# Kernel optimization log

Hardware: AMD Instinct MI355X
Metric: run time of the kernel (lower is better)

## Reference

```python
import jax, jax.numpy as jnp
import numpy as np

CK, CV, CS = 8, 120, 64          # key / value / spatial-basis channels
NUM_AGENTS, NQ_PER = 4, 4        # queries chunked per agent; chunk(a,4) hard-codes NQ_PER=4
HID = 256                        # lstm_hidden_size
NA = 18                          # num_actions
U = 8                            # Fourier freqs; CS = U*U = 64
MLP_W = 512                      # q/a mlp hidden width


def spatial_basis(h, w):
    # fixed (h, w, CS) cos-product Fourier basis (SpatialBasis buffer)
    ph = jnp.arange(1, h + 1, dtype=jnp.float32)[:, None] * jnp.ones((1, w), jnp.float32) * (np.pi / h)
    pw = jnp.ones((h, 1), jnp.float32) * jnp.arange(1, w + 1, dtype=jnp.float32)[None, :] * (np.pi / w)
    u = jnp.arange(1, U + 1, dtype=jnp.float32)
    ca = jnp.cos(ph[..., None] * u)   # (h, w, U)
    cb = jnp.cos(pw[..., None] * u)   # (h, w, U)
    return jnp.einsum('hwu,hwv->hwuv', ca, cb).reshape(h, w, U * U)


def mlp3(x, w0, b0, w1, b1, w2, b2):
    # build_mlp with 2 relu hidden layers + identity output
    x = jax.nn.relu(x @ w0 + b0)
    x = jax.nn.relu(x @ w1 + b1)
    return x @ w2 + b2


def lstm_cell(x, h, c, w_ih, w_hh, b_ih, b_hh):
    gates = x @ w_ih.T + b_ih + h @ w_hh.T + b_hh
    i, f, g, o = jnp.split(gates, 4, axis=1)
    c2 = jax.nn.sigmoid(f) * c + jax.nn.sigmoid(i) * jnp.tanh(g)
    return jax.nn.sigmoid(o) * jnp.tanh(c2), c2


def setup_inputs() -> dict:
    key = jax.random.key(0)
    ks = jax.random.split(key, 24)
    n, h, w = 128, 64, 64
    s = 0.02
    nq = NUM_AGENTS * NQ_PER
    q_out = nq * (CK + CS)                       # 1152
    a_in = NQ_PER * (CK + 2 * CS + CV) + 2       # 1026
    r = lambda k, shp: jax.random.normal(k, shp, jnp.float32)
    return {
        'x': r(ks[0], (n, h, w, CK + CV)),
        'c': 1,
        'r_prev': r(ks[1], (n,)),
        'a_prev': r(ks[2], (n,)),
        'prev_hidden': r(ks[3], (n, HID)),
        'prev_cell': r(ks[4], (n, HID)),
        'q_w0': r(ks[5], (HID, MLP_W)) * s, 'q_b0': jnp.zeros((MLP_W,), jnp.float32),
        'q_w1': r(ks[6], (MLP_W, MLP_W)) * s, 'q_b1': jnp.zeros((MLP_W,), jnp.float32),
        'q_w2': r(ks[7], (MLP_W, q_out)) * s, 'q_b2': jnp.zeros((q_out,), jnp.float32),
        'a_w0': r(ks[8], (a_in, MLP_W)) * s, 'a_b0': jnp.zeros((MLP_W,), jnp.float32),
        'a_w1': r(ks[9], (MLP_W, MLP_W)) * s, 'a_b1': jnp.zeros((MLP_W,), jnp.float32),
        'a_w2': r(ks[10], (MLP_W, HID)) * s, 'a_b2': jnp.zeros((HID,), jnp.float32),
        'w_ih': r(ks[11], (4 * HID, HID)) * s, 'w_hh': r(ks[12], (4 * HID, HID)) * s,
        'b_ih': jnp.zeros((4 * HID,), jnp.float32), 'b_hh': jnp.zeros((4 * HID,), jnp.float32),
        'p_w': r(ks[13], (HID, NA)) * s, 'p_b': jnp.zeros((NA,), jnp.float32),
        'v_w': r(ks[14], (HID, NA)) * s, 'v_b': jnp.zeros((NA,), jnp.float32),
    }


def reference(x, c, r_prev, a_prev, prev_hidden, prev_cell,
              q_w0, q_b0, q_w1, q_b1, q_w2, q_b2,
              a_w0, a_b0, a_w1, a_b1, a_w2, a_b2,
              w_ih, w_hh, b_ih, b_hh, p_w, p_b, v_w, v_b):
    n, h, w, _ = x.shape
    S = spatial_basis(h, w)
    Sb = jnp.broadcast_to(S, (n, h, w, CS))
    K = jnp.concatenate([x[..., :CK], Sb], axis=-1)   # (n,h,w,CK+CS)
    V = jnp.concatenate([x[..., CK:], Sb], axis=-1)   # (n,h,w,CV+CS)
    # queries from previous hidden state, take agent c's chunk
    Q = mlp3(prev_hidden, q_w0, q_b0, q_w1, q_b1, q_w2, q_b2)
    Q = Q.reshape(n, NUM_AGENTS * NQ_PER, CK + CS)[:, c * NQ_PER:(c + 1) * NQ_PER, :]  # (n,4,CK+CS)
    # spatial QK attention with softmax over the h*w grid
    A = jnp.einsum('nhwd,nqd->nhwq', K, Q)            # (n,h,w,4)
    A = jax.nn.softmax(A.reshape(n, h * w, NQ_PER), axis=1).reshape(n, h, w, NQ_PER)
    a = jnp.einsum('nhwq,nhwd->nqd', A, V)            # (n,4,CV+CS)
    # concat answers + queries + prev reward/action scalars
    answer = jnp.concatenate([a.reshape(n, -1), Q.reshape(n, -1),
                              r_prev[:, None], a_prev[:, None]], axis=1)  # (n,1026)
    answer = mlp3(answer, a_w0, a_b0, a_w1, a_b1, a_w2, a_b2)             # (n,HID)
    hN, _cN = lstm_cell(answer, prev_hidden, prev_cell, w_ih, w_hh, b_ih, b_hh)
    logits = hN @ p_w + p_b
    values = hN @ v_w + v_b
    return logits, values
```

## Files before the change

### kernel.cpp

```cpp
#include <hip/hip_runtime.h>
#include <math.h>

#define NTOT   128
#define NPOS   4096
#define PVCH   16
#define PVLEN  256
#define LCH    8
#define LCLEN  512

__global__ __launch_bounds__(256) void k_gemm(
    const float* __restrict__ Ad, const float* __restrict__ pA,
    const float* __restrict__ biasA, int nzA, int reluA,
    const float* __restrict__ pvR, const float* __restrict__ scl,
    const float* __restrict__ W, float* __restrict__ pbuf,
    int N, int K, int ldw, int gkc, const int* __restrict__ cptr, int cmul) {
  __shared__ float Xs[4][128];
  const int t  = threadIdx.x;
  const int j  = blockIdx.x * 256 + t;
  const int m0 = blockIdx.y * 4;
  const int k0 = blockIdx.z * gkc;
  const int klen = min(gkc, K - k0);
  const int coff = cptr[0] * cmul;

  for (int idx = t; idx < 4 * klen; idx += 256) {
    int mi = idx / klen;
    int kk = idx - mi * klen;
    int col = k0 + kk;
    float s;
    if (Ad) {
      bool pv = false;
      int q = 0, d = 0;
      if (pvR && col < 736) {
        q = col / 184; d = col - q * 184;
        pv = (d < 120);
      }
      if (pv) {
        const size_t eo = (size_t)(m0 + mi) * 480 + q * 120 + d;
        float s0 = 0.f, s1 = 0.f, s2 = 0.f, s3 = 0.f;
#pragma unroll
        for (int c = 0; c < PVCH; c += 4) {
          s0 += pvR[(size_t)((c + 0) * NTOT) * 480 + eo];
          s1 += pvR[(size_t)((c + 1) * NTOT) * 480 + eo];
          s2 += pvR[(size_t)((c + 2) * NTOT) * 480 + eo];
          s3 += pvR[(size_t)((c + 3) * NTOT) * 480 + eo];
        }
        s = ((s0 + s1) + (s2 + s3)) * scl[(size_t)(m0 + mi) * 4 + q];
      } else {
        s = Ad[(size_t)(m0 + mi) * K + col];
      }
    } else {
      float s0 = biasA[col], s1 = 0.f, s2 = 0.f, s3 = 0.f;
      int z = 0;
      for (; z + 4 <= nzA; z += 4) {
        s0 += pA[((size_t)(z + 0) * NTOT + m0 + mi) * K + col];
        s1 += pA[((size_t)(z + 1) * NTOT + m0 + mi) * K + col];
        s2 += pA[((size_t)(z + 2) * NTOT + m0 + mi) * K + col];
        s3 += pA[((size_t)(z + 3) * NTOT + m0 + mi) * K + col];
      }
      for (; z < nzA; ++z) s0 += pA[((size_t)z * NTOT + m0 + mi) * K + col];
      s = (s0 + s1) + (s2 + s3);
      if (reluA) s = fmaxf(s, 0.f);
    }
    Xs[mi][kk] = s;
  }
  __syncthreads();

  if (j < N) {
    float acc[4];
#pragma unroll
    for (int mi = 0; mi < 4; ++mi) acc[mi] = 0.f;
    const float* wp = W + (size_t)k0 * ldw + coff + j;
#pragma unroll 16
    for (int kk = 0; kk < klen; ++kk) {
      float wv = wp[(size_t)kk * ldw];
#pragma unroll
      for (int mi = 0; mi < 4; ++mi) acc[mi] = fmaf(Xs[mi][kk], wv, acc[mi]);
    }
    float* op = pbuf + ((size_t)blockIdx.z * NTOT + m0) * N + j;
#pragma unroll
    for (int mi = 0; mi < 4; ++mi) op[(size_t)mi * N] = acc[mi];
  }
}

__global__ __launch_bounds__(512) void k_logits(
    const float* __restrict__ x, const float* __restrict__ pQ,
    const float* __restrict__ q_b2, const int* __restrict__ cptr,
    const float* __restrict__ r_prev, const float* __restrict__ a_prev,
    float* __restrict__ Pw, float* __restrict__ Lpart,
    float* __restrict__ rsum, float* __restrict__ ans) {
  const int ck = blockIdx.x;
  const int n  = blockIdx.y;
  const int t  = threadIdx.x;
  const int wave = t >> 6, lane = t & 63;

  __shared__ float Qs[4][72];
  __shared__ float ct[64][8];
  __shared__ float cbQ[4 * 576];
  __shared__ float4 wlds[LCLEN];
  __shared__ float red[4][8];

  const float PI64 = 3.14159265358979323846f / 64.f;

  if (t < 288) {
    const int coff = cptr[0] * 288;
    float s = q_b2[coff + t];
#pragma unroll
    for (int z = 0; z < 8; ++z) s += pQ[((size_t)z * NTOT + n) * 288 + t];
    Qs[t / 72][t % 72] = s;
  }
  {
    int i = t >> 3, u = t & 7;
    ct[i][u] = cosf((float)((i + 1) * (u + 1)) * PI64);
  }
  __syncthreads();

  for (int e = t; e < 2048; e += 512) {
    int q = e >> 9, j = (e >> 3) & 63, u = e & 7;
    float s = 0.f;
#pragma unroll
    for (int v = 0; v < 8; ++v) s += ct[j][v] * Qs[q][8 + u * 8 + v];
    cbQ[q * 576 + j * 9 + u] = s;
  }
  __syncthreads();

  const int base = ck * LCLEN;
  const float* xp = x + (size_t)n * NPOS * 128;

  const int irow = ck * 8 + wave;
  {
    const int pos = base + t;
    const float4* xr = reinterpret_cast<const float4*>(xp + (size_t)pos * 128);
    float4 xa = xr[0], xb = xr[1];
    float4 w;
    float lg[4];
#pragma unroll
    for (int q = 0; q < 4; ++q) {
      float s = xa.x * Qs[q][0] + xa.y * Qs[q][1] + xa.z * Qs[q][2] + xa.w * Qs[q][3]
              + xb.x * Qs[q][4] + xb.y * Qs[q][5] + xb.z * Qs[q][6] + xb.w * Qs[q][7];
      const float* cq = cbQ + q * 576 + lane * 9;
      float s2 = 0.f;
#pragma unroll
      for (int u = 0; u < 8; ++u) s2 += ct[irow][u] * cq[u];
      lg[q] = s + s2;
    }
    w.x = __expf(lg[0]); w.y = __expf(lg[1]);
    w.z = __expf(lg[2]); w.w = __expf(lg[3]);
    wlds[t] = w;
    reinterpret_cast<float4*>(Pw)[(size_t)n * NPOS + base + t] = w;

    float lsum[4] = {w.x, w.y, w.z, w.w};
#pragma unroll
    for (int off = 32; off; off >>= 1)
#pragma unroll
      for (int q = 0; q < 4; ++q) lsum[q] += __shfl_xor(lsum[q], off);
    if (lane == 0)
#pragma unroll
      for (int q = 0; q < 4; ++q) red[q][wave] = lsum[q];
  }
  __syncthreads();
  if (t < 4) {
    float s = 0.f;
#pragma unroll
    for (int w8 = 0; w8 < 8; ++w8) s += red[t][w8];
    Lpart[((size_t)n * LCH + ck) * 4 + t] = s;
  }

  if (t < 256) {
    int i = t >> 5, q = (t >> 3) & 3, v = t & 7;
    const float* wb = reinterpret_cast<const float*>(&wlds[i * 64]) + q;
    float s0 = 0.f, s1 = 0.f, s2 = 0.f, s3 = 0.f;
#pragma unroll 8
    for (int j = 0; j < 64; j += 4) {
      s0 += wb[(j + 0) * 4] * ct[j + 0][v];
      s1 += wb[(j + 1) * 4] * ct[j + 1][v];
      s2 += wb[(j + 2) * 4] * ct[j + 2][v];
      s3 += wb[(j + 3) * 4] * ct[j + 3][v];
    }
    rsum[((size_t)n * 64 + ck * 8 + i) * 32 + q * 8 + v] = (s0 + s1) + (s2 + s3);
  }

  if (ck == 0) {
    float* ap = ans + (size_t)n * 1026;
    if (t < 288) ap[736 + t] = Qs[t / 72][t % 72];
    if (t == 288) { ap[1024] = r_prev[n]; ap[1025] = a_prev[n]; }
  }
}

__global__ __launch_bounds__(256, 4) void k_pv(
    const float* __restrict__ x, const float* __restrict__ Pw,
    const float* __restrict__ Lpart, const float* __restrict__ rsum,
    float* __restrict__ pvp, float* __restrict__ scl, float* __restrict__ ans) {
  const int n = blockIdx.y, ck = blockIdx.x;
  const int t = threadIdx.x, wave = t >> 6, lane = t & 63;
  __shared__ float4 wl[PVLEN];
  __shared__ __align__(16) float part[4][4][120];
  __shared__ float ct2[64][8];
  __shared__ float sc_s[4];

  const int base = ck * PVLEN;
  wl[t] = reinterpret_cast<const float4*>(Pw)[(size_t)n * NPOS + base + t];
  __syncthreads();

  const int xl = (lane < 60) ? lane : 59;
  const float* vb = x + ((size_t)n * NPOS + base + wave * 64) * 128 + 8 + 2 * xl;

  float ax0[4] = {0.f, 0.f, 0.f, 0.f};
  float ax1[4] = {0.f, 0.f, 0.f, 0.f};
#pragma unroll
  for (int b = 0; b < 4; ++b) {
    float2 v0  = *reinterpret_cast<const float2*>(vb + (size_t)(b * 16 + 0)  * 128);
    float2 v1  = *reinterpret_cast<const float2*>(vb + (size_t)(b * 16 + 1)  * 128);
    float2 v2  = *reinterpret_cast<const float2*>(vb + (size_t)(b * 16 + 2)  * 128);
    float2 v3  = *reinterpret_cast<const float2*>(vb + (size_t)(b * 16 + 3)  * 128);
    float2 v4  = *reinterpret_cast<const float2*>(vb + (size_t)(b * 16 + 4)  * 128);
    float2 v5  = *reinterpret_cast<const float2*>(vb + (size_t)(b * 16 + 5)  * 128);
    float2 v6  = *reinterpret_cast<const float2*>(vb + (size_t)(b * 16 + 6)  * 128);
    float2 v7  = *reinterpret_cast<const float2*>(vb + (size_t)(b * 16 + 7)  * 128);
    float2 v8  = *reinterpret_cast<const float2*>(vb + (size_t)(b * 16 + 8)  * 128);
    float2 v9  = *reinterpret_cast<const float2*>(vb + (size_t)(b * 16 + 9)  * 128);
    float2 v10 = *reinterpret_cast<const float2*>(vb + (size_t)(b * 16 + 10) * 128);
    float2 v11 = *reinterpret_cast<const float2*>(vb + (size_t)(b * 16 + 11) * 128);
    float2 v12 = *reinterpret_cast<const float2*>(vb + (size_t)(b * 16 + 12) * 128);
    float2 v13 = *reinterpret_cast<const float2*>(vb + (size_t)(b * 16 + 13) * 128);
    float2 v14 = *reinterpret_cast<const float2*>(vb + (size_t)(b * 16 + 14) * 128);
    float2 v15 = *reinterpret_cast<const float2*>(vb + (size_t)(b * 16 + 15) * 128);
#define ACC(VV, II)                                                              \
    {                                                                            \
      float4 w = wl[wave * 64 + b * 16 + II];                                    \
      ax0[0] += w.x * VV.x; ax1[0] += w.x * VV.y;                                \
      ax0[1] += w.y * VV.x; ax1[1] += w.y * VV.y;                                \
      ax0[2] += w.z * VV.x; ax1[2] += w.z * VV.y;                                \
      ax0[3] += w.w * VV.x; ax1[3] += w.w * VV.y;                                \
    }
    ACC(v0, 0)  ACC(v1, 1)  ACC(v2, 2)  ACC(v3, 3)
    ACC(v4, 4)  ACC(v5, 5)  ACC(v6, 6)  ACC(v7, 7)
    ACC(v8, 8)  ACC(v9, 9)  ACC(v10, 10) ACC(v11, 11)
    ACC(v12, 12) ACC(v13, 13) ACC(v14, 14) ACC(v15, 15)
#undef ACC
  }
  if (lane < 60) {
#pragma unroll
    for (int q = 0; q < 4; ++q)
      *reinterpret_cast<float2*>(&part[wave][q][2 * lane]) = make_float2(ax0[q], ax1[q]);
  }
  __syncthreads();

  float* op = pvp + ((size_t)ck * NTOT + n) * 480;
  for (int idx = t; idx < 480; idx += 256) {
    const int q = idx / 120, d = idx - q * 120;
    op[idx] = (part[0][q][d] + part[1][q][d]) + (part[2][q][d] + part[3][q][d]);
  }

  if (ck == 0) {
    const float PI64 = 3.14159265358979323846f / 64.f;
    if (t < 4) {
      float L = 0.f;
#pragma unroll
      for (int c = 0; c < LCH; ++c) L += Lpart[((size_t)n * LCH + c) * 4 + t];
      float s = 1.f / L;
      scl[(size_t)n * 4 + t] = s;
      sc_s[t] = s;
    }
    for (int e = t; e < 512; e += 256) {
      int i = e >> 3, u = e & 7;
      ct2[i][u] = cosf((float)((i + 1) * (u + 1)) * PI64);
    }
    __syncthreads();
    {
      const int q = t >> 6, uv = t & 63, u = uv >> 3, v = uv & 7;
      const float* rp = rsum + (size_t)n * 64 * 32 + q * 8 + v;
      float s0 = 0.f, s1 = 0.f, s2 = 0.f, s3 = 0.f;
#pragma unroll 8
      for (int row = 0; row < 64; row += 4) {
        s0 += ct2[row + 0][u] * rp[(row + 0) * 32];
        s1 += ct2[row + 1][u] * rp[(row + 1) * 32];
        s2 += ct2[row + 2][u] * rp[(row + 2) * 32];
        s3 += ct2[row + 3][u] * rp[(row + 3) * 32];
      }
      ans[(size_t)n * 1026 + q * 184 + 120 + uv] = sc_s[q] * ((s0 + s1) + (s2 + s3));
    }
  }
}

__global__ __launch_bounds__(256) void k_gates(
    const float* __restrict__ pA, const float* __restrict__ biasA,
    const float* __restrict__ hp,
    const float* __restrict__ w_ih, const float* __restrict__ w_hh,
    const float* __restrict__ b_ih, const float* __restrict__ b_hh,
    float* __restrict__ gbuf) {
  const int t = threadIdx.x;
  const int n0 = blockIdx.x * 2;
  const int r0 = blockIdx.y * 64;
  __shared__ float xs[2][256], hs[2][256];
  __shared__ float red[64][4][5];
#pragma unroll
  for (int s = 0; s < 2; ++s) {
    float v0 = biasA[t], v1 = 0.f, v2 = 0.f, v3 = 0.f;
#pragma unroll
    for (int z = 0; z < 8; z += 4) {
      v0 += pA[((size_t)(z + 0) * NTOT + n0 + s) * 256 + t];
      v1 += pA[((size_t)(z + 1) * NTOT + n0 + s) * 256 + t];
      v2 += pA[((size_t)(z + 2) * NTOT + n0 + s) * 256 + t];
      v3 += pA[((size_t)(z + 3) * NTOT + n0 + s) * 256 + t];
    }
    xs[s][t] = (v0 + v1) + (v2 + v3);
    hs[s][t] = hp[(size_t)(n0 + s) * 256 + t];
  }
  __syncthreads();
  const int r = t >> 2, kq = t & 3;
  const int row = r0 + r;
  const float4* wi = reinterpret_cast<const float4*>(w_ih + (size_t)row * 256 + kq * 64);
  const float4* wh = reinterpret_cast<const float4*>(w_hh + (size_t)row * 256 + kq * 64);
  float s00 = 0.f, s01 = 0.f, s10 = 0.f, s11 = 0.f;
#pragma unroll
  for (int i = 0; i < 16; ++i) {
    float4 a = wi[i], b = wh[i];
    const int k4 = kq * 64 + i * 4;
    s00 += a.x * xs[0][k4] + a.y * xs[0][k4 + 1] + a.z * xs[0][k4 + 2] + a.w * xs[0][k4 + 3];
    s01 += a.x * xs[1][k4] + a.y * xs[1][k4 + 1] + a.z * xs[1][k4 + 2] + a.w * xs[1][k4 + 3];
    s10 += b.x * hs[0][k4] + b.y * hs[0][k4 + 1] + b.z * hs[0][k4 + 2] + b.w * hs[0][k4 + 3];
    s11 += b.x * hs[1][k4] + b.y * hs[1][k4 + 1] + b.z * hs[1][k4 + 2] + b.w * hs[1][k4 + 3];
  }
  red[r][kq][0] = s00; red[r][kq][1] = s01; red[r][kq][2] = s10; red[r][kq][3] = s11;
  __syncthreads();
  if (t < 128) {
    const int rr = t >> 1, s = t & 1;
    float g = b_ih[r0 + rr] + b_hh[r0 + rr];
#pragma unroll
    for (int k = 0; k < 4; ++k) g += red[rr][k][s] + red[rr][k][2 + s];
    gbuf[(size_t)(n0 + s) * 1024 + r0 + rr] = g;
  }
}

__global__ __launch_bounds__(256) void k_lstm2(
    const float* __restrict__ gbuf, const float* __restrict__ cp,
    const float* __restrict__ p_w, const float* __restrict__ p_b,
    const float* __restrict__ v_w, const float* __restrict__ v_b,
    float* __restrict__ out) {
  const int t = threadIdx.x;
  const int n0 = blockIdx.x * 2;
  __shared__ float h2[2][256];
#pragma unroll
  for (int s = 0; s < 2; ++s) {
    const size_t gb = (size_t)(n0 + s) * 1024;
    float gi = gbuf[gb + t], gf = gbuf[gb + 256 + t];
    float gg = gbuf[gb + 512 + t], go = gbuf[gb + 768 + t];
    float si = 1.f / (1.f + __expf(-gi));
    float sf = 1.f / (1.f + __expf(-gf));
    float so = 1.f / (1.f + __expf(-go));
    float c2 = sf * cp[(size_t)(n0 + s) * 256 + t] + si * tanhf(gg);
    h2[s][t] = so * tanhf(c2);
  }
  __syncthreads();
  if (t < 72) {
    const int si = t / 36, r = t % 36, iv = r / 18, j = r % 18;
    const float* W = iv ? v_w : p_w;
    const float* B = iv ? v_b : p_b;
    float s = B[j];
#pragma unroll 8
    for (int k = 0; k < 256; ++k) s += h2[si][k] * W[k * 18 + j];
    out[(size_t)iv * (NTOT * 18) + (size_t)(n0 + si) * 18 + j] = s;
  }
}

extern "C" void kernel_launch(void* const* d_in, const int* in_sizes, int n_in,
                              void* d_out, int out_size, void* d_ws, size_t ws_size,
                              hipStream_t stream) {
  const float* x      = (const float*)d_in[0];
  const int*   cptr   = (const int*)d_in[1];
  const float* r_prev = (const float*)d_in[2];
  const float* a_prev = (const float*)d_in[3];
  const float* hprev  = (const float*)d_in[4];
  const float* cprev  = (const float*)d_in[5];
  const float* q_w0 = (const float*)d_in[6];
  const float* q_b0 = (const float*)d_in[7];
  const float* q_w1 = (const float*)d_in[8];
  const float* q_b1 = (const float*)d_in[9];
  const float* q_w2 = (const float*)d_in[10];
  const float* q_b2 = (const float*)d_in[11];
  const float* a_w0 = (const float*)d_in[12];
  const float* a_b0 = (const float*)d_in[13];
  const float* a_w1 = (const float*)d_in[14];
  const float* a_b1 = (const float*)d_in[15];
  const float* a_w2 = (const float*)d_in[16];
  const float* a_b2 = (const float*)d_in[17];
  const float* w_ih = (const float*)d_in[18];
  const float* w_hh = (const float*)d_in[19];
  const float* b_ih = (const float*)d_in[20];
  const float* b_hh = (const float*)d_in[21];
  const float* p_w  = (const float*)d_in[22];
  const float* p_b  = (const float*)d_in[23];
  const float* v_w  = (const float*)d_in[24];
  const float* v_b  = (const float*)d_in[25];
  float* out = (float*)d_out;
  float* ws  = (float*)d_ws;

  float* pQ   = ws;
  float* pb1  = pQ   + 294912;
  float* pb2  = pb1  + 589824;
  float* pb3  = pb2  + 524288;
  float* Pw   = pb3  + 262144;
  float* pvp  = Pw   + 2097152;
  float* ans  = pvp  + 983040;
  float* gbuf = ans  + 131328;
  float* Lp   = gbuf + 131072;
  float* rsum = Lp   + 4096;
  float* scl  = rsum + 262144;

  k_gemm<<<dim3(2, 32, 4), 256, 0, stream>>>(hprev, nullptr, nullptr, 0, 0, nullptr, nullptr,
                                             q_w0, pb1, 512, 256, 512, 64, cptr, 0);
  k_gemm<<<dim3(2, 32, 8), 256, 0, stream>>>(nullptr, pb1, q_b0, 4, 1, nullptr, nullptr,
                                             q_w1, pb2, 512, 512, 512, 64, cptr, 0);
  k_gemm<<<dim3(2, 32, 8), 256, 0, stream>>>(nullptr, pb2, q_b1, 8, 1, nullptr, nullptr,
                                             q_w2, pQ, 288, 512, 1152, 64, cptr, 288);

  k_logits<<<dim3(LCH, NTOT), 512, 0, stream>>>(x, pQ, q_b2, cptr, r_prev, a_prev,
                                                Pw, Lp, rsum, ans);
  k_pv<<<dim3(PVCH, NTOT), 256, 0, stream>>>(x, Pw, Lp, rsum, pvp, scl, ans);

  k_gemm<<<dim3(2, 32, 9), 256, 0, stream>>>(ans, nullptr, nullptr, 0, 0, pvp, scl,
                                             a_w0, pb1, 512, 1026, 512, 128, cptr, 0);
  k_gemm<<<dim3(2, 32, 8), 256, 0, stream>>>(nullptr, pb1, a_b0, 9, 1, nullptr, nullptr,
                                             a_w1, pb2, 512, 512, 512, 64, cptr, 0);
  k_gemm<<<dim3(1, 32, 8), 256, 0, stream>>>(nullptr, pb2, a_b1, 8, 1, nullptr, nullptr,
                                             a_w2, pb3, 256, 512, 256, 64, cptr, 0);

  k_gates<<<dim3(64, 16), 256, 0, stream>>>(pb3, a_b2, hprev, w_ih, w_hh, b_ih, b_hh, gbuf);
  k_lstm2<<<64, 256, 0, stream>>>(gbuf, cprev, p_w, p_b, v_w, v_b, out);
}
```

Measured before the change: 133.4 us.

## Fuse logits and PV into one attention kernel, drop Pw round-trip

The logits kernel and the PV-accumulation kernel are merged so the exponentiated weights stay in shared memory. This removes the global write and re-read of the weight buffer and a second pass over x. The cross-chunk finalisation moves into a small separate kernel. Each block now handles 512 positions with 8 waves instead of 256 positions, so there are fewer, larger blocks. Shared memory is reused between cbQ and the partial sums.

```diff
diff --git a/kernel.cpp b/kernel.cpp
--- a/kernel.cpp
+++ b/kernel.cpp
@@ -3,8 +3,7 @@
 
 #define NTOT   128
 #define NPOS   4096
-#define PVCH   16
-#define PVLEN  256
+#define PVCH   8
 #define LCH    8
 #define LCLEN  512
 
@@ -82,11 +81,11 @@
   }
 }
 
-__global__ __launch_bounds__(512) void k_logits(
+__global__ __launch_bounds__(512) void k_attn(
     const float* __restrict__ x, const float* __restrict__ pQ,
     const float* __restrict__ q_b2, const int* __restrict__ cptr,
     const float* __restrict__ r_prev, const float* __restrict__ a_prev,
-    float* __restrict__ Pw, float* __restrict__ Lpart,
+    float* __restrict__ pvp, float* __restrict__ Lpart,
     float* __restrict__ rsum, float* __restrict__ ans) {
   const int ck = blockIdx.x;
   const int n  = blockIdx.y;
@@ -95,9 +94,11 @@
 
   __shared__ float Qs[4][72];
   __shared__ float ct[64][8];
-  __shared__ float cbQ[4 * 576];
   __shared__ float4 wlds[LCLEN];
   __shared__ float red[4][8];
+  __shared__ __align__(16) float uni[3840];
+  float* cbQ = uni;
+  float (*part)[4][120] = reinterpret_cast<float (*)[4][120]>(uni);
 
   const float PI64 = 3.14159265358979323846f / 64.f;
 
@@ -125,8 +126,8 @@
 
   const int base = ck * LCLEN;
   const float* xp = x + (size_t)n * NPOS * 128;
-
   const int irow = ck * 8 + wave;
+
   {
     const int pos = base + t;
     const float4* xr = reinterpret_cast<const float4*>(xp + (size_t)pos * 128);
@@ -146,7 +147,6 @@
     w.x = __expf(lg[0]); w.y = __expf(lg[1]);
     w.z = __expf(lg[2]); w.w = __expf(lg[3]);
     wlds[t] = w;
-    reinterpret_cast<float4*>(Pw)[(size_t)n * NPOS + base + t] = w;
 
     float lsum[4] = {w.x, w.y, w.z, w.w};
 #pragma unroll
@@ -165,44 +165,8 @@
     Lpart[((size_t)n * LCH + ck) * 4 + t] = s;
   }
 
-  if (t < 256) {
-    int i = t >> 5, q = (t >> 3) & 3, v = t & 7;
-    const float* wb = reinterpret_cast<const float*>(&wlds[i * 64]) + q;
-    float s0 = 0.f, s1 = 0.f, s2 = 0.f, s3 = 0.f;
-#pragma unroll 8
-    for (int j = 0; j < 64; j += 4) {
-      s0 += wb[(j + 0) * 4] * ct[j + 0][v];
-      s1 += wb[(j + 1) * 4] * ct[j + 1][v];
-      s2 += wb[(j + 2) * 4] * ct[j + 2][v];
-      s3 += wb[(j + 3) * 4] * ct[j + 3][v];
-    }
-    rsum[((size_t)n * 64 + ck * 8 + i) * 32 + q * 8 + v] = (s0 + s1) + (s2 + s3);
-  }
-
-  if (ck == 0) {
-    float* ap = ans + (size_t)n * 1026;
-    if (t < 288) ap[736 + t] = Qs[t / 72][t % 72];
-    if (t == 288) { ap[1024] = r_prev[n]; ap[1025] = a_prev[n]; }
-  }
-}
-
-__global__ __launch_bounds__(256, 4) void k_pv(
-    const float* __restrict__ x, const float* __restrict__ Pw,
-    const float* __restrict__ Lpart, const float* __restrict__ rsum,
-    float* __restrict__ pvp, float* __restrict__ scl, float* __restrict__ ans) {
-  const int n = blockIdx.y, ck = blockIdx.x;
-  const int t = threadIdx.x, wave = t >> 6, lane = t & 63;
-  __shared__ float4 wl[PVLEN];
-  __shared__ __align__(16) float part[4][4][120];
-  __shared__ float ct2[64][8];
-  __shared__ float sc_s[4];
-
-  const int base = ck * PVLEN;
-  wl[t] = reinterpret_cast<const float4*>(Pw)[(size_t)n * NPOS + base + t];
-  __syncthreads();
-
   const int xl = (lane < 60) ? lane : 59;
-  const float* vb = x + ((size_t)n * NPOS + base + wave * 64) * 128 + 8 + 2 * xl;
+  const float* vb = xp + (size_t)(base + wave * 64) * 128 + 8 + 2 * xl;
 
   float ax0[4] = {0.f, 0.f, 0.f, 0.f};
   float ax1[4] = {0.f, 0.f, 0.f, 0.f};
@@ -226,7 +190,7 @@
     float2 v15 = *reinterpret_cast<const float2*>(vb + (size_t)(b * 16 + 15) * 128);
 #define ACC(VV, II)                                                              \
     {                                                                            \
-      float4 w = wl[wave * 64 + b * 16 + II];                                    \
+      float4 w = wlds[wave * 64 + b * 16 + II];                                  \
       ax0[0] += w.x * VV.x; ax1[0] += w.x * VV.y;                                \
       ax0[1] += w.y * VV.x; ax1[1] += w.y * VV.y;                                \
       ax0[2] += w.z * VV.x; ax1[2] += w.z * VV.y;                                \
@@ -245,40 +209,72 @@
   }
   __syncthreads();
 
-  float* op = pvp + ((size_t)ck * NTOT + n) * 480;
-  for (int idx = t; idx < 480; idx += 256) {
-    const int q = idx / 120, d = idx - q * 120;
-    op[idx] = (part[0][q][d] + part[1][q][d]) + (part[2][q][d] + part[3][q][d]);
+  {
+    float* op = pvp + ((size_t)ck * NTOT + n) * 480;
+    if (t < 480) {
+      const int q = t / 120, d = t - q * 120;
+      float s0 = part[0][q][d] + part[1][q][d];
+      float s1 = part[2][q][d] + part[3][q][d];
+      float s2 = part[4][q][d] + part[5][q][d];
+      float s3 = part[6][q][d] + part[7][q][d];
+      op[t] = (s0 + s1) + (s2 + s3);
+    }
+  }
+
+  if (t < 256) {
+    int i = t >> 5, q = (t >> 3) & 3, v = t & 7;
+    const float* wb = reinterpret_cast<const float*>(&wlds[i * 64]) + q;
+    float s0 = 0.f, s1 = 0.f, s2 = 0.f, s3 = 0.f;
+#pragma unroll 8
+    for (int j = 0; j < 64; j += 4) {
+      s0 += wb[(j + 0) * 4] * ct[j + 0][v];
+      s1 += wb[(j + 1) * 4] * ct[j + 1][v];
+      s2 += wb[(j + 2) * 4] * ct[j + 2][v];
+      s3 += wb[(j + 3) * 4] * ct[j + 3][v];
+    }
+    rsum[((size_t)n * 64 + ck * 8 + i) * 32 + q * 8 + v] = (s0 + s1) + (s2 + s3);
   }
 
   if (ck == 0) {
-    const float PI64 = 3.14159265358979323846f / 64.f;
-    if (t < 4) {
-      float L = 0.f;
-#pragma unroll
-      for (int c = 0; c < LCH; ++c) L += Lpart[((size_t)n * LCH + c) * 4 + t];
-      float s = 1.f / L;
-      scl[(size_t)n * 4 + t] = s;
-      sc_s[t] = s;
-    }
-    for (int e = t; e < 512; e += 256) {
-      int i = e >> 3, u = e & 7;
-      ct2[i][u] = cosf((float)((i + 1) * (u + 1)) * PI64);
-    }
-    __syncthreads();
-    {
-      const int q = t >> 6, uv = t & 63, u = uv >> 3, v = uv & 7;
-      const float* rp = rsum + (size_t)n * 64 * 32 + q * 8 + v;
-      float s0 = 0.f, s1 = 0.f, s2 = 0.f, s3 = 0.f;
+    float* ap = ans + (size_t)n * 1026;
+    if (t >= 480 && t < 480 + 288) ap[736 + (t - 480)] = Qs[(t - 480) / 72][(t - 480) % 72];
+    if (t == 479) { ap[1024] = r_prev[n]; ap[1025] = a_prev[n]; }
+  }
+}
+
+__global__ __launch_bounds__(256) void k_fin(
+    const float* __restrict__ Lpart, const float* __restrict__ rsum,
+    float* __restrict__ scl, float* __restrict__ ans) {
+  const int n = blockIdx.x, t = threadIdx.x;
+  __shared__ float ct2[64][8];
+  __shared__ float sc_s[4];
+  const float PI64 = 3.14159265358979323846f / 64.f;
+
+  if (t < 4) {
+    float L = 0.f;
+#pragma unroll
+    for (int c = 0; c < LCH; ++c) L += Lpart[((size_t)n * LCH + c) * 4 + t];
+    float s = 1.f / L;
+    scl[(size_t)n * 4 + t] = s;
+    sc_s[t] = s;
+  }
+  for (int e = t; e < 512; e += 256) {
+    int i = e >> 3, u = e & 7;
+    ct2[i][u] = cosf((float)((i + 1) * (u + 1)) * PI64);
+  }
+  __syncthreads();
+  {
+    const int q = t >> 6, uv = t & 63, u = uv >> 3, v = uv & 7;
+    const float* rp = rsum + (size_t)n * 64 * 32 + q * 8 + v;
+    float s0 = 0.f, s1 = 0.f, s2 = 0.f, s3 = 0.f;
 #pragma unroll 8
-      for (int row = 0; row < 64; row += 4) {
-        s0 += ct2[row + 0][u] * rp[(row + 0) * 32];
-        s1 += ct2[row + 1][u] * rp[(row + 1) * 32];
-        s2 += ct2[row + 2][u] * rp[(row + 2) * 32];
-        s3 += ct2[row + 3][u] * rp[(row + 3) * 32];
-      }
-      ans[(size_t)n * 1026 + q * 184 + 120 + uv] = sc_s[q] * ((s0 + s1) + (s2 + s3));
-    }
+    for (int row = 0; row < 64; row += 4) {
+      s0 += ct2[row + 0][u] * rp[(row + 0) * 32];
+      s1 += ct2[row + 1][u] * rp[(row + 1) * 32];
+      s2 += ct2[row + 2][u] * rp[(row + 2) * 32];
+      s3 += ct2[row + 3][u] * rp[(row + 3) * 32];
+    }
+    ans[(size_t)n * 1026 + q * 184 + 120 + uv] = sc_s[q] * ((s0 + s1) + (s2 + s3));
   }
 }
 
@@ -399,9 +395,8 @@
   float* pb1  = pQ   + 294912;
   float* pb2  = pb1  + 589824;
   float* pb3  = pb2  + 524288;
-  float* Pw   = pb3  + 262144;
-  float* pvp  = Pw   + 2097152;
-  float* ans  = pvp  + 983040;
+  float* pvp  = pb3  + 262144;
+  float* ans  = pvp  + 491520;
   float* gbuf = ans  + 131328;
   float* Lp   = gbuf + 131072;
   float* rsum = Lp   + 4096;
@@ -414,9 +409,9 @@
   k_gemm<<<dim3(2, 32, 8), 256, 0, stream>>>(nullptr, pb2, q_b1, 8, 1, nullptr, nullptr,
                                              q_w2, pQ, 288, 512, 1152, 64, cptr, 288);
 
-  k_logits<<<dim3(LCH, NTOT), 512, 0, stream>>>(x, pQ, q_b2, cptr, r_prev, a_prev,
-                                                Pw, Lp, rsum, ans);
-  k_pv<<<dim3(PVCH, NTOT), 256, 0, stream>>>(x, Pw, Lp, rsum, pvp, scl, ans);
+  k_attn<<<dim3(LCH, NTOT), 512, 0, stream>>>(x, pQ, q_b2, cptr, r_prev, a_prev,
+                                              pvp, Lp, rsum, ans);
+  k_fin<<<NTOT, 256, 0, stream>>>(Lp, rsum, scl, ans);
 
   k_gemm<<<dim3(2, 32, 9), 256, 0, stream>>>(ans, nullptr, nullptr, 0, 0, pvp, scl,
                                              a_w0, pb1, 512, 1026, 512, 128, cptr, 0);
```

After: 132.7 us. Within noise of the previous version (-0.5%).
